# Performance work log

Hardware: AMD Instinct MI355X
Metric: run time of the kernel (lower is better)

## Reference

```python
import jax, jax.numpy as jnp
import numpy as np

N_NODES = 50000
N_EDGES = 800000
IN_FEATS = 256
OUT_FEATS = 32
NUM_HEADS = 8
NEG_SLOPE = 0.2


def setup_inputs() -> dict:
    key = jax.random.key(0)
    k_feat, k_src, k_dst, k_w, k_al, k_ar = jax.random.split(key, 6)
    feat = jax.random.normal(k_feat, (N_NODES, IN_FEATS), dtype=jnp.float32)
    src = jax.random.randint(k_src, (N_EDGES,), 0, N_NODES)
    dst = jax.random.randint(k_dst, (N_EDGES,), 0, N_NODES)
    # fc weight, stored as [in, H*F] so projection is feat @ W
    W = jax.random.normal(k_w, (IN_FEATS, NUM_HEADS * OUT_FEATS), dtype=jnp.float32) * 0.05
    attn_l = jax.random.normal(k_al, (NUM_HEADS, OUT_FEATS), dtype=jnp.float32) * 0.1
    attn_r = jax.random.normal(k_ar, (NUM_HEADS, OUT_FEATS), dtype=jnp.float32) * 0.1
    bias = jnp.zeros((NUM_HEADS, OUT_FEATS), dtype=jnp.float32)
    return {"feat": feat, "W": W, "attn_l": attn_l, "attn_r": attn_r,
            "bias": bias, "src": src, "dst": dst}


def reference(feat, W, attn_l, attn_r, bias, src, dst):
    N = feat.shape[0]
    H, F = attn_l.shape
    # node projection: [N, H, F]
    h = (feat @ W).reshape(N, H, F)
    # per-node attention logits (source code uses feat_src for both el and er)
    el = jnp.einsum('nhf,hf->nh', h, attn_l)  # [N, H]
    er = jnp.einsum('nhf,hf->nh', h, attn_r)  # [N, H]
    # per-edge logit: u_add_v then LeakyReLU
    e = el[src] + er[dst]                      # [E, H]
    e = jnp.where(e > 0, e, NEG_SLOPE * e)
    # edge softmax normalized over incoming edges of each dst node
    m = jax.ops.segment_max(e, dst, num_segments=N)   # [N, H], -inf for 0-deg
    ex = jnp.exp(e - m[dst])                           # [E, H]
    s = jax.ops.segment_sum(ex, dst, num_segments=N)   # [N, H]
    a = ex / s[dst]                                     # [E, H]
    # weighted scatter-sum aggregation: u_mul_e -> sum
    msg = h[src] * a[:, :, None]                        # [E, H, F]
    rst = jax.ops.segment_sum(msg, dst, num_segments=N)  # [N, H, F]
    rst = rst + bias[None, :, :]
    return rst
```

## Files before the change

### kernel.cpp

```cpp
#include <hip/hip_runtime.h>
#include <math.h>

#define NN 50000
#define NE 800000
#define IN_F 256
#define HF 256
#define NH 8
#define NEG_SLOPE 0.2f
#define CAP 64

#define GEMM_BLOCKS 782
#define EDGE_BLOCKS 3125
#define ELR_BLOCKS 12500
#define AGG_BLOCKS 3125
#define ZERO_BLOCKS 196

typedef short bf16x8 __attribute__((ext_vector_type(8)));
typedef float f32x16 __attribute__((ext_vector_type(16)));

__device__ __forceinline__ unsigned short f2bf(float x) {
    unsigned u = __float_as_uint(x);
    u += 0x7FFF + ((u >> 16) & 1);
    return (unsigned short)(u >> 16);
}
__device__ __forceinline__ float bf2f(unsigned short b) {
    return __uint_as_float(((unsigned)b) << 16);
}

__global__ __launch_bounds__(256) void wconv_zero_kernel(const float* __restrict__ W,
                                                         unsigned short* __restrict__ Wb,
                                                         int* __restrict__ cnt) {
    int bid = blockIdx.x;
    if (bid < 256) {
        int e = bid * 256 + threadIdx.x;
        int k = e >> 8, n = e & 255;
        float x = W[e];
        int kt = k >> 5, kk = k & 31;
        Wb[((size_t)(kt * 256 + n)) * 32 + kk] = f2bf(x);
    } else {
        int i = (bid - 256) * 256 + threadIdx.x;
        if (i < NN) cnt[i] = 0;
    }
}

__global__ void fill2_kernel(const int* __restrict__ src, const int* __restrict__ dst,
                             int* __restrict__ cnt, unsigned short* __restrict__ slots) {
    int e = blockIdx.x * 256 + threadIdx.x;
    if (e < NE) {
        int d = dst[e];
        int pos = atomicAdd(&cnt[d], 1);
        if (pos < CAP) slots[(size_t)d * CAP + pos] = (unsigned short)src[e];
    }
}

__global__ __launch_bounds__(256) void gemm_kernel(const float* __restrict__ feat,
                                                   const unsigned short* __restrict__ Wb,
                                                   unsigned short* __restrict__ h, int M) {
    __shared__ __align__(16) unsigned short As_hi[2][64][40];

    const int tid = threadIdx.x;
    const int lane = tid & 63;
    const int wid = tid >> 6;
    const int bm = blockIdx.x * 64;

    const int arow = tid >> 2;
    const int achk = tid & 3;
    const int grow = bm + arow;
    const int crow = (grow < M) ? grow : 0;
    const float* ap = feat + (size_t)crow * IN_F + achk * 8;

    f32x16 acc[2][2];
    #pragma unroll
    for (int mi = 0; mi < 2; ++mi)
        #pragma unroll
        for (int ni = 0; ni < 2; ++ni)
            #pragma unroll
            for (int r = 0; r < 16; ++r) acc[mi][ni][r] = 0.f;

    const int khalf = lane >> 5;
    const int nbase = wid * 64 + (lane & 31);
    const unsigned short* wb0 = Wb + (size_t)nbase * 32 + khalf * 8;

    float4 cur0 = *(const float4*)(ap);
    float4 cur1 = *(const float4*)(ap + 4);

    bf16x8 bhc[2][2];
    #pragma unroll
    for (int ksc = 0; ksc < 2; ++ksc)
        #pragma unroll
        for (int ni = 0; ni < 2; ++ni)
            bhc[ksc][ni] = *(const bf16x8*)(wb0 + ni * 1024 + ksc * 16);

    for (int kt = 0; kt < 8; ++kt) {
        const int buf = kt & 1;
        float4 nxt0, nxt1;
        bf16x8 bhn[2][2];
        if (kt < 7) {
            nxt0 = *(const float4*)(ap + (kt + 1) * 32);
            nxt1 = *(const float4*)(ap + (kt + 1) * 32 + 4);
            const unsigned short* wbn = wb0 + (size_t)(kt + 1) * 8192;
            #pragma unroll
            for (int ksc = 0; ksc < 2; ++ksc)
                #pragma unroll
                for (int ni = 0; ni < 2; ++ni)
                    bhn[ksc][ni] = *(const bf16x8*)(wbn + ni * 1024 + ksc * 16);
        }

        float xs[8] = {cur0.x, cur0.y, cur0.z, cur0.w, cur1.x, cur1.y, cur1.z, cur1.w};
        unsigned hi2[4];
        #pragma unroll
        for (int p = 0; p < 4; ++p) {
            unsigned short h0 = f2bf(xs[2 * p]), h1 = f2bf(xs[2 * p + 1]);
            hi2[p] = (unsigned)h0 | ((unsigned)h1 << 16);
        }
        *(int4*)&As_hi[buf][arow][achk * 8] = make_int4(hi2[0], hi2[1], hi2[2], hi2[3]);
        __syncthreads();

        #pragma unroll
        for (int ksc = 0; ksc < 2; ++ksc) {
            const int kchunk = ksc * 2 + khalf;
            bf16x8 ah[2];
            #pragma unroll
            for (int mi = 0; mi < 2; ++mi) {
                int r = mi * 32 + (lane & 31);
                ah[mi] = *(const bf16x8*)&As_hi[buf][r][kchunk * 8];
            }
            #pragma unroll
            for (int mi = 0; mi < 2; ++mi)
                #pragma unroll
                for (int ni = 0; ni < 2; ++ni)
                    acc[mi][ni] = __builtin_amdgcn_mfma_f32_32x32x16_bf16(ah[mi], bhc[ksc][ni], acc[mi][ni], 0, 0, 0);
        }
        cur0 = nxt0;
        cur1 = nxt1;
        #pragma unroll
        for (int ksc = 0; ksc < 2; ++ksc)
            #pragma unroll
            for (int ni = 0; ni < 2; ++ni)
                bhc[ksc][ni] = bhn[ksc][ni];
    }

    #pragma unroll
    for (int mi = 0; mi < 2; ++mi)
        #pragma unroll
        for (int ni = 0; ni < 2; ++ni)
            #pragma unroll
            for (int r = 0; r < 16; ++r) {
                int row = mi * 32 + (r & 3) + 8 * (r >> 2) + 4 * (lane >> 5);
                int col = wid * 64 + ni * 32 + (lane & 31);
                int gr = bm + row;
                if (gr < M) h[(size_t)gr * HF + col] = f2bf(acc[mi][ni][r]);
            }
}

__global__ __launch_bounds__(256) void elr_kernel(const unsigned short* __restrict__ h,
                                                  const float* __restrict__ al,
                                                  const float* __restrict__ ar,
                                                  float* __restrict__ el,
                                                  float* __restrict__ er) {
    int node = blockIdx.x * 4 + (threadIdx.x >> 6);
    if (node >= NN) return;
    int lane = threadIdx.x & 63;
    short4 hv = *(const short4*)&h[(size_t)node * HF + lane * 4];
    float h0 = bf2f((unsigned short)hv.x), h1 = bf2f((unsigned short)hv.y);
    float h2 = bf2f((unsigned short)hv.z), h3 = bf2f((unsigned short)hv.w);
    float4 alv = *(const float4*)&al[lane * 4];
    float4 arv = *(const float4*)&ar[lane * 4];
    float pl = h0 * alv.x + h1 * alv.y + h2 * alv.z + h3 * alv.w;
    float pr = h0 * arv.x + h1 * arv.y + h2 * arv.z + h3 * arv.w;
    #pragma unroll
    for (int off = 1; off < 8; off <<= 1) {
        pl += __shfl_xor(pl, off);
        pr += __shfl_xor(pr, off);
    }
    if ((lane & 7) == 0) {
        el[node * NH + (lane >> 3)] = pl;
        er[node * NH + (lane >> 3)] = pr;
    }
}

__global__ __launch_bounds__(256) void agg_kernel(const unsigned short* __restrict__ h,
                                                  const float* __restrict__ el,
                                                  const float* __restrict__ er,
                                                  const int* __restrict__ cnt,
                                                  const unsigned short* __restrict__ slots,
                                                  const float* __restrict__ bias,
                                                  float* __restrict__ out) {
    int wv = blockIdx.x * 4 + (threadIdx.x >> 6);
    int lane = threadIdx.x & 63;
    int eg = lane >> 3;
    int fg = lane & 7;
    int e2 = (lane >> 5) & 1, e1 = (lane >> 4) & 1, e0 = (lane >> 3) & 1;
    int col = fg * 32 + eg * 4;
    float4 bv = *(const float4*)&bias[col];

    int4 deg4 = *(const int4*)&cnt[wv * 4];

    #pragma unroll 1
    for (int t = 0; t < 4; ++t) {
        int node = wv * 4 + t;
        int deg = (t == 0) ? deg4.x : (t == 1) ? deg4.y : (t == 2) ? deg4.z : deg4.w;
        deg = deg < CAP ? deg : CAP;
        const unsigned short* sl = slots + (size_t)node * CAP;
        float er_mine = er[(size_t)node * NH + fg];

        float ssum = 0.f;
        float acc[32];
        #pragma unroll
        for (int j = 0; j < 32; ++j) acc[j] = 0.f;

        for (int i0 = 0; i0 < deg; i0 += 16) {
            int idxA = i0 + eg;
            int idxB = i0 + 8 + eg;
            bool vA = idxA < deg, vB = idxB < deg;
            int sA = sl[vA ? idxA : 0];
            int sB = sl[vB ? idxB : 0];
            float eA = el[(size_t)sA * NH + fg] + er_mine;
            float eB = el[(size_t)sB * NH + fg] + er_mine;
            eA = eA > 0.f ? eA : NEG_SLOPE * eA;
            eB = eB > 0.f ? eB : NEG_SLOPE * eB;
            float pA = vA ? __expf(eA) : 0.f;
            float pB = vB ? __expf(eB) : 0.f;
            ssum += pA + pB;
            const unsigned short* hpA = h + (size_t)sA * HF + fg * 32;
            const unsigned short* hpB = h + (size_t)sB * HF + fg * 32;
            bf16x8 va[4], vb[4];
            #pragma unroll
            for (int c = 0; c < 4; ++c) { va[c] = *(const bf16x8*)(hpA + c * 8); }
            #pragma unroll
            for (int c = 0; c < 4; ++c) { vb[c] = *(const bf16x8*)(hpB + c * 8); }
            #pragma unroll
            for (int c = 0; c < 4; ++c)
                #pragma unroll
                for (int k = 0; k < 8; ++k) {
                    acc[c * 8 + k] = fmaf(bf2f((unsigned short)va[c][k]), pA, acc[c * 8 + k]);
                    acc[c * 8 + k] = fmaf(bf2f((unsigned short)vb[c][k]), pB, acc[c * 8 + k]);
                }
        }

        ssum += __shfl_xor(ssum, 8);
        ssum += __shfl_xor(ssum, 16);
        ssum += __shfl_xor(ssum, 32);
        float inv_s = (ssum > 0.f) ? 1.f / ssum : 0.f;

        float t16[16];
        #pragma unroll
        for (int j = 0; j < 16; ++j) {
            float keep = e2 ? acc[16 + j] : acc[j];
            float send = e2 ? acc[j] : acc[16 + j];
            t16[j] = keep + __shfl_xor(send, 32);
        }
        float t8[8];
        #pragma unroll
        for (int j = 0; j < 8; ++j) {
            float keep = e1 ? t16[8 + j] : t16[j];
            float send = e1 ? t16[j] : t16[8 + j];
            t8[j] = keep + __shfl_xor(send, 16);
        }
        float t4[4];
        #pragma unroll
        for (int j = 0; j < 4; ++j) {
            float keep = e0 ? t8[4 + j] : t8[j];
            float send = e0 ? t8[j] : t8[4 + j];
            t4[j] = keep + __shfl_xor(send, 8);
        }

        float4 o = make_float4(fmaf(t4[0], inv_s, bv.x), fmaf(t4[1], inv_s, bv.y),
                               fmaf(t4[2], inv_s, bv.z), fmaf(t4[3], inv_s, bv.w));
        *(float4*)&out[(size_t)node * HF + col] = o;
    }
}

extern "C" void kernel_launch(void* const* d_in, const int* in_sizes, int n_in,
                              void* d_out, int out_size, void* d_ws, size_t ws_size,
                              hipStream_t stream) {
    const float* feat = (const float*)d_in[0];
    const float* W    = (const float*)d_in[1];
    const float* al   = (const float*)d_in[2];
    const float* ar   = (const float*)d_in[3];
    const float* bias = (const float*)d_in[4];
    const int*   src  = (const int*)d_in[5];
    const int*   dst  = (const int*)d_in[6];
    float* out = (float*)d_out;

    char* ws = (char*)d_ws;
    size_t off = 0;
    unsigned short* h = (unsigned short*)(ws + off);     off += (size_t)NN * HF * 2;
    float* el = (float*)(ws + off);                      off += (size_t)NN * NH * 4;
    float* er = (float*)(ws + off);                      off += (size_t)NN * NH * 4;
    int* cnt = (int*)(ws + off);                         off += (size_t)NN * 4;
    unsigned short* slots = (unsigned short*)(ws + off); off += (size_t)NN * CAP * 2;
    unsigned short* Wb = (unsigned short*)(ws + off);    off += (size_t)IN_F * HF * 2;

    wconv_zero_kernel<<<256 + ZERO_BLOCKS, 256, 0, stream>>>(W, Wb, cnt);
    fill2_kernel<<<EDGE_BLOCKS, 256, 0, stream>>>(src, dst, cnt, slots);
    gemm_kernel<<<GEMM_BLOCKS, 256, 0, stream>>>(feat, Wb, h, NN);
    elr_kernel<<<ELR_BLOCKS, 256, 0, stream>>>(h, al, ar, el, er);
    agg_kernel<<<AGG_BLOCKS, 256, 0, stream>>>(h, el, er, cnt, slots, bias, out);
}
```

Measured before the change: 153.8 us.

## Fold attention vectors into weights and compute el/er inside GEMM

Precomputes W·attn_l and W·attn_r as a small extra bf16 weight block, then computes el/er with an extra MFMA per k-step inside the projection GEMM. This removes the separate elr kernel, which re-read the whole bf16 h tensor and cost a launch. In exchange the GEMM does some redundant MFMA work in every wave, and el/er are now computed from bf16-rounded folded weights rather than from rounded h, which shifts numerics slightly.

```diff
diff --git a/kernel.cpp b/kernel.cpp
--- a/kernel.cpp
+++ b/kernel.cpp
@@ -11,9 +11,9 @@
 
 #define GEMM_BLOCKS 782
 #define EDGE_BLOCKS 3125
-#define ELR_BLOCKS 12500
 #define AGG_BLOCKS 3125
 #define ZERO_BLOCKS 196
+#define WALR_BLOCKS 16
 
 typedef short bf16x8 __attribute__((ext_vector_type(8)));
 typedef float f32x16 __attribute__((ext_vector_type(16)));
@@ -28,7 +28,10 @@
 }
 
 __global__ __launch_bounds__(256) void wconv_zero_kernel(const float* __restrict__ W,
+                                                         const float* __restrict__ al,
+                                                         const float* __restrict__ ar,
                                                          unsigned short* __restrict__ Wb,
+                                                         unsigned short* __restrict__ Wb2,
                                                          int* __restrict__ cnt) {
     int bid = blockIdx.x;
     if (bid < 256) {
@@ -37,9 +40,21 @@
         float x = W[e];
         int kt = k >> 5, kk = k & 31;
         Wb[((size_t)(kt * 256 + n)) * 32 + kk] = f2bf(x);
-    } else {
+    } else if (bid < 256 + ZERO_BLOCKS) {
         int i = (bid - 256) * 256 + threadIdx.x;
         if (i < NN) cnt[i] = 0;
+    } else {
+        int idx = (bid - 256 - ZERO_BLOCKS) * 256 + threadIdx.x;
+        int k = idx >> 4, c = idx & 15;
+        int ch = c & 7;
+        const float* av = (c < 8) ? al : ar;
+        float s = 0.f;
+        #pragma unroll
+        for (int f = 0; f < 32; ++f)
+            s = fmaf(W[(size_t)k * 256 + ch * 32 + f], av[ch * 32 + f], s);
+        int kt = k >> 5, kk = k & 31;
+        Wb2[(kt * 32 + c) * 32 + kk] = f2bf(s);
+        Wb2[(kt * 32 + 16 + c) * 32 + kk] = 0;
     }
 }
 
@@ -55,7 +70,10 @@
 
 __global__ __launch_bounds__(256) void gemm_kernel(const float* __restrict__ feat,
                                                    const unsigned short* __restrict__ Wb,
-                                                   unsigned short* __restrict__ h, int M) {
+                                                   const unsigned short* __restrict__ Wb2,
+                                                   unsigned short* __restrict__ h,
+                                                   float* __restrict__ el,
+                                                   float* __restrict__ er, int M) {
     __shared__ __align__(16) unsigned short As_hi[2][64][40];
 
     const int tid = threadIdx.x;
@@ -76,10 +94,14 @@
         for (int ni = 0; ni < 2; ++ni)
             #pragma unroll
             for (int r = 0; r < 16; ++r) acc[mi][ni][r] = 0.f;
+    f32x16 acc_e;
+    #pragma unroll
+    for (int r = 0; r < 16; ++r) acc_e[r] = 0.f;
 
     const int khalf = lane >> 5;
     const int nbase = wid * 64 + (lane & 31);
     const unsigned short* wb0 = Wb + (size_t)nbase * 32 + khalf * 8;
+    const unsigned short* wb2base = Wb2 + (size_t)(lane & 31) * 32 + khalf * 8;
 
     float4 cur0 = *(const float4*)(ap);
     float4 cur1 = *(const float4*)(ap + 4);
@@ -130,6 +152,8 @@
                 #pragma unroll
                 for (int ni = 0; ni < 2; ++ni)
                     acc[mi][ni] = __builtin_amdgcn_mfma_f32_32x32x16_bf16(ah[mi], bhc[ksc][ni], acc[mi][ni], 0, 0, 0);
+            bf16x8 be = *(const bf16x8*)(wb2base + kt * 1024 + ksc * 16);
+            acc_e = __builtin_amdgcn_mfma_f32_32x32x16_bf16(ah[wid & 1], be, acc_e, 0, 0, 0);
         }
         cur0 = nxt0;
         cur1 = nxt1;
@@ -151,31 +175,18 @@
                 int gr = bm + row;
                 if (gr < M) h[(size_t)gr * HF + col] = f2bf(acc[mi][ni][r]);
             }
-}
-
-__global__ __launch_bounds__(256) void elr_kernel(const unsigned short* __restrict__ h,
-                                                  const float* __restrict__ al,
-                                                  const float* __restrict__ ar,
-                                                  float* __restrict__ el,
-                                                  float* __restrict__ er) {
-    int node = blockIdx.x * 4 + (threadIdx.x >> 6);
-    if (node >= NN) return;
-    int lane = threadIdx.x & 63;
-    short4 hv = *(const short4*)&h[(size_t)node * HF + lane * 4];
-    float h0 = bf2f((unsigned short)hv.x), h1 = bf2f((unsigned short)hv.y);
-    float h2 = bf2f((unsigned short)hv.z), h3 = bf2f((unsigned short)hv.w);
-    float4 alv = *(const float4*)&al[lane * 4];
-    float4 arv = *(const float4*)&ar[lane * 4];
-    float pl = h0 * alv.x + h1 * alv.y + h2 * alv.z + h3 * alv.w;
-    float pr = h0 * arv.x + h1 * arv.y + h2 * arv.z + h3 * arv.w;
-    #pragma unroll
-    for (int off = 1; off < 8; off <<= 1) {
-        pl += __shfl_xor(pl, off);
-        pr += __shfl_xor(pr, off);
-    }
-    if ((lane & 7) == 0) {
-        el[node * NH + (lane >> 3)] = pl;
-        er[node * NH + (lane >> 3)] = pr;
+
+    if (wid < 2) {
+        const int col = lane & 31;
+        #pragma unroll
+        for (int r = 0; r < 16; ++r) {
+            int row = wid * 32 + (r & 3) + 8 * (r >> 2) + 4 * (lane >> 5);
+            int gr = bm + row;
+            if (gr < M) {
+                if (col < 8)       el[(size_t)gr * NH + col] = acc_e[r];
+                else if (col < 16) er[(size_t)gr * NH + (col - 8)] = acc_e[r];
+            }
+        }
     }
 }
 
@@ -291,10 +302,10 @@
     int* cnt = (int*)(ws + off);                         off += (size_t)NN * 4;
     unsigned short* slots = (unsigned short*)(ws + off); off += (size_t)NN * CAP * 2;
     unsigned short* Wb = (unsigned short*)(ws + off);    off += (size_t)IN_F * HF * 2;
-
-    wconv_zero_kernel<<<256 + ZERO_BLOCKS, 256, 0, stream>>>(W, Wb, cnt);
+    unsigned short* Wb2 = (unsigned short*)(ws + off);   off += (size_t)8 * 32 * 32 * 2;
+
+    wconv_zero_kernel<<<256 + ZERO_BLOCKS + WALR_BLOCKS, 256, 0, stream>>>(W, al, ar, Wb, Wb2, cnt);
     fill2_kernel<<<EDGE_BLOCKS, 256, 0, stream>>>(src, dst, cnt, slots);
-    gemm_kernel<<<GEMM_BLOCKS, 256, 0, stream>>>(feat, Wb, h, NN);
-    elr_kernel<<<ELR_BLOCKS, 256, 0, stream>>>(h, al, ar, el, er);
+    gemm_kernel<<<GEMM_BLOCKS, 256, 0, stream>>>(feat, Wb, Wb2, h, el, er, NN);
     agg_kernel<<<AGG_BLOCKS, 256, 0, stream>>>(h, el, er, cnt, slots, bias, out);
 }
```

Result: slower. 176.1 us (+14.5%).
